# Kernel tuning notes

Measured on AMD Instinct MI355X. Metric: run time of the kernel, lower is better.

## Reference

```python
import jax, jax.numpy as jnp
import numpy as np

B, N, DIM, HEADS = 2, 2048, 1024, 16
DH = DIM // HEADS
SCALE = DH ** -0.5


def setup_inputs() -> dict:
    key = jax.random.key(0)
    k1, k2, k3, k4 = jax.random.split(key, 4)
    x = jax.random.normal(k1, (B, N, DIM), dtype=jnp.float32)
    # nn.Linear weights stored as [out, in]; apply as x @ W.T
    w_qkv = jax.random.normal(k2, (3 * DIM, DIM), dtype=jnp.float32) * (DIM ** -0.5)
    w_out = jax.random.normal(k3, (DIM, DIM), dtype=jnp.float32) * (DIM ** -0.5)
    b_out = jax.random.normal(k4, (DIM,), dtype=jnp.float32) * 0.01
    return {"x": x, "w_qkv": w_qkv, "w_out": w_out, "b_out": b_out}


def reference(x, w_qkv, w_out, b_out):
    b, n, _ = x.shape
    qkv = jnp.einsum('bnd,ed->bne', x, w_qkv)  # [b, n, 3*dim]
    q, k, v = jnp.split(qkv, 3, axis=-1)
    # [b, n, dim] -> [b, heads, n, dim_head]
    def split_heads(t):
        return t.reshape(b, n, HEADS, DH).transpose(0, 2, 1, 3)
    q, k, v = split_heads(q), split_heads(k), split_heads(v)
    attn = jnp.einsum('bhid,bhjd->bhij', q, k) * SCALE  # [b, h, n, n]
    attn = jax.nn.softmax(attn, axis=-1)
    out = jnp.einsum('bhij,bhjd->bhid', attn, v)  # [b, h, n, dh]
    out = out.transpose(0, 2, 1, 3).reshape(b, n, DIM)
    return jnp.einsum('bnd,ed->bne', out, w_out) + b_out
```

## Files before the change

### kernel.cpp

```cpp
#include <hip/hip_runtime.h>
#include <hip/hip_bf16.h>
#include <stdint.h>

#define BB 2
#define NN 2048
#define DIMM 1024
#define HEADS 16
#define DH 64
#define E3 3072
#define LOG2E_ 1.44269504088896f
#define THR_ 8.0f

typedef __bf16 bf16;
typedef __attribute__((ext_vector_type(8))) __bf16 bf16x8;
typedef __attribute__((ext_vector_type(4))) __bf16 bf16x4;
typedef __attribute__((ext_vector_type(4))) float f32x4;

__device__ __forceinline__ void gload_lds16(const void* gsrc, void* ldst) {
  __builtin_amdgcn_global_load_lds(
      (const __attribute__((address_space(1))) uint32_t*)(uintptr_t)gsrc,
      (__attribute__((address_space(3))) uint32_t*)(uintptr_t)ldst,
      16, 0, 0);
}

__global__ __launch_bounds__(256)
void convert_all(const float* __restrict__ x, const float* __restrict__ wqkv,
                 const float* __restrict__ wout,
                 bf16* __restrict__ xb, bf16* __restrict__ wqb, bf16* __restrict__ wob) {
  size_t i = (size_t)blockIdx.x * blockDim.x + threadIdx.x;
  const float* src;
  bf16* dst;
  size_t off;
  if (i < 1048576u) { src = x; dst = xb; off = i; }
  else if (i < 1048576u + 786432u) { src = wqkv; dst = wqb; off = i - 1048576u; }
  else { src = wout; dst = wob; off = i - (1048576u + 786432u); }
  float4 v = ((const float4*)src)[off];
  bf16x4 o;
  o[0] = (bf16)v.x; o[1] = (bf16)v.y; o[2] = (bf16)v.z; o[3] = (bf16)v.w;
  *(bf16x4*)(dst + off * 4) = o;
}

#define GDSR(dst, base, off) \
  asm volatile("ds_read_b128 %0, %1 offset:%c2" : "=v"(dst) : "v"(base), "i"(off))

#define GRD12(ABASE, BBASE, OFF) \
  GDSR(af0, ABASE, (OFF));        GDSR(af1, ABASE, (OFF)+2048); \
  GDSR(af2, ABASE, (OFF)+4096);   GDSR(af3, ABASE, (OFF)+6144); \
  GDSR(af4, ABASE, (OFF)+8192);   GDSR(af5, ABASE, (OFF)+10240); \
  GDSR(af6, ABASE, (OFF)+12288);  GDSR(af7, ABASE, (OFF)+14336); \
  GDSR(bf0, BBASE, (OFF));        GDSR(bf1, BBASE, (OFF)+2048); \
  GDSR(bf2, BBASE, (OFF)+4096);   GDSR(bf3, BBASE, (OFF)+6144);

#define GMM32() \
  acc[0][0]=__builtin_amdgcn_mfma_f32_16x16x32_bf16(af0,bf0,acc[0][0],0,0,0); \
  acc[0][1]=__builtin_amdgcn_mfma_f32_16x16x32_bf16(af0,bf1,acc[0][1],0,0,0); \
  acc[0][2]=__builtin_amdgcn_mfma_f32_16x16x32_bf16(af0,bf2,acc[0][2],0,0,0); \
  acc[0][3]=__builtin_amdgcn_mfma_f32_16x16x32_bf16(af0,bf3,acc[0][3],0,0,0); \
  acc[1][0]=__builtin_amdgcn_mfma_f32_16x16x32_bf16(af1,bf0,acc[1][0],0,0,0); \
  acc[1][1]=__builtin_amdgcn_mfma_f32_16x16x32_bf16(af1,bf1,acc[1][1],0,0,0); \
  acc[1][2]=__builtin_amdgcn_mfma_f32_16x16x32_bf16(af1,bf2,acc[1][2],0,0,0); \
  acc[1][3]=__builtin_amdgcn_mfma_f32_16x16x32_bf16(af1,bf3,acc[1][3],0,0,0); \
  acc[2][0]=__builtin_amdgcn_mfma_f32_16x16x32_bf16(af2,bf0,acc[2][0],0,0,0); \
  acc[2][1]=__builtin_amdgcn_mfma_f32_16x16x32_bf16(af2,bf1,acc[2][1],0,0,0); \
  acc[2][2]=__builtin_amdgcn_mfma_f32_16x16x32_bf16(af2,bf2,acc[2][2],0,0,0); \
  acc[2][3]=__builtin_amdgcn_mfma_f32_16x16x32_bf16(af2,bf3,acc[2][3],0,0,0); \
  acc[3][0]=__builtin_amdgcn_mfma_f32_16x16x32_bf16(af3,bf0,acc[3][0],0,0,0); \
  acc[3][1]=__builtin_amdgcn_mfma_f32_16x16x32_bf16(af3,bf1,acc[3][1],0,0,0); \
  acc[3][2]=__builtin_amdgcn_mfma_f32_16x16x32_bf16(af3,bf2,acc[3][2],0,0,0); \
  acc[3][3]=__builtin_amdgcn_mfma_f32_16x16x32_bf16(af3,bf3,acc[3][3],0,0,0); \
  acc[4][0]=__builtin_amdgcn_mfma_f32_16x16x32_bf16(af4,bf0,acc[4][0],0,0,0); \
  acc[4][1]=__builtin_amdgcn_mfma_f32_16x16x32_bf16(af4,bf1,acc[4][1],0,0,0); \
  acc[4][2]=__builtin_amdgcn_mfma_f32_16x16x32_bf16(af4,bf2,acc[4][2],0,0,0); \
  acc[4][3]=__builtin_amdgcn_mfma_f32_16x16x32_bf16(af4,bf3,acc[4][3],0,0,0); \
  acc[5][0]=__builtin_amdgcn_mfma_f32_16x16x32_bf16(af5,bf0,acc[5][0],0,0,0); \
  acc[5][1]=__builtin_amdgcn_mfma_f32_16x16x32_bf16(af5,bf1,acc[5][1],0,0,0); \
  acc[5][2]=__builtin_amdgcn_mfma_f32_16x16x32_bf16(af5,bf2,acc[5][2],0,0,0); \
  acc[5][3]=__builtin_amdgcn_mfma_f32_16x16x32_bf16(af5,bf3,acc[5][3],0,0,0); \
  acc[6][0]=__builtin_amdgcn_mfma_f32_16x16x32_bf16(af6,bf0,acc[6][0],0,0,0); \
  acc[6][1]=__builtin_amdgcn_mfma_f32_16x16x32_bf16(af6,bf1,acc[6][1],0,0,0); \
  acc[6][2]=__builtin_amdgcn_mfma_f32_16x16x32_bf16(af6,bf2,acc[6][2],0,0,0); \
  acc[6][3]=__builtin_amdgcn_mfma_f32_16x16x32_bf16(af6,bf3,acc[6][3],0,0,0); \
  acc[7][0]=__builtin_amdgcn_mfma_f32_16x16x32_bf16(af7,bf0,acc[7][0],0,0,0); \
  acc[7][1]=__builtin_amdgcn_mfma_f32_16x16x32_bf16(af7,bf1,acc[7][1],0,0,0); \
  acc[7][2]=__builtin_amdgcn_mfma_f32_16x16x32_bf16(af7,bf2,acc[7][2],0,0,0); \
  acc[7][3]=__builtin_amdgcn_mfma_f32_16x16x32_bf16(af7,bf3,acc[7][3],0,0,0);

#define GSTAGE(BUF) { \
  gload_lds16(pA,          smem + (BUF)*32768 + w*1024); \
  gload_lds16(pA + 65536,  smem + (BUF)*32768 + 8192 + w*1024); \
  gload_lds16(pA + 131072, smem + (BUF)*32768 + 16384 + w*1024); \
  gload_lds16(pA + 196608, smem + (BUF)*32768 + 24576 + w*1024); \
  gload_lds16(pB,          smem + 65536 + (BUF)*32768 + w*1024); \
  gload_lds16(pB + 65536,  smem + 65536 + (BUF)*32768 + 8192 + w*1024); \
  gload_lds16(pB + 131072, smem + 65536 + (BUF)*32768 + 16384 + w*1024); \
  gload_lds16(pB + 196608, smem + 65536 + (BUF)*32768 + 24576 + w*1024); \
  pA += 64; pB += 64; }

#define GSTEP(BUF, DOSTAGE) { \
  bf16x8 af0, af1, af2, af3, af4, af5, af6, af7, bf0, bf1, bf2, bf3; \
  GRD12(abase0, bbase0, (BUF)*32768); \
  if (DOSTAGE) { GSTAGE((BUF)^1); } \
  asm volatile("s_waitcnt lgkmcnt(0)" ::: "memory"); \
  __builtin_amdgcn_sched_barrier(0); \
  __builtin_amdgcn_s_setprio(1); \
  GMM32(); \
  __builtin_amdgcn_s_setprio(0); \
  GRD12(abase1, bbase1, (BUF)*32768); \
  asm volatile("s_waitcnt lgkmcnt(0)" ::: "memory"); \
  __builtin_amdgcn_sched_barrier(0); \
  __builtin_amdgcn_s_setprio(1); \
  GMM32(); \
  __builtin_amdgcn_s_setprio(0); \
  if (DOSTAGE) { asm volatile("s_waitcnt vmcnt(0)" ::: "memory"); } \
  __builtin_amdgcn_sched_barrier(0); \
  __builtin_amdgcn_s_barrier(); \
}

__global__ __launch_bounds__(512, 2)
void gemm_qkv(const bf16* __restrict__ A, const bf16* __restrict__ Bw,
              bf16* __restrict__ C) {
  int bid = blockIdx.x;
  bid = (bid & 7) * 24 + (bid >> 3);
  const int nx = bid % 12;
  const int ny = bid / 12;
  const int m0 = ny * 256, n0 = nx * 256;
  const int tid = threadIdx.x;
  const int w = tid >> 6, lane = tid & 63, c = lane & 15, g = lane >> 4;
  const int wr = w >> 2, wc = w & 3;

  __shared__ __align__(16) char smem[131072];
  const uint32_t smem32 = (uint32_t)(uintptr_t)smem;
  const uint32_t abase0 = smem32 + (wr * 128 + c) * 128 + ((g ^ (c & 7)) * 16);
  const uint32_t abase1 = smem32 + (wr * 128 + c) * 128 + (((4 + g) ^ (c & 7)) * 16);
  const uint32_t bbase0 = smem32 + 65536 + (wc * 64 + c) * 128 + ((g ^ (c & 7)) * 16);
  const uint32_t bbase1 = smem32 + 65536 + (wc * 64 + c) * 128 + (((4 + g) ^ (c & 7)) * 16);

  const bf16 *pA, *pB;
  {
    const int r0 = tid >> 3;
    const int cc = (tid & 7) ^ ((tid >> 3) & 7);
    pA = A + (size_t)(m0 + r0) * 1024 + cc * 8;
    pB = Bw + (size_t)(n0 + r0) * 1024 + cc * 8;
  }

  f32x4 acc[8][4] = {};

  GSTAGE(0);
  asm volatile("s_waitcnt vmcnt(0)" ::: "memory");
  __builtin_amdgcn_sched_barrier(0);
  __builtin_amdgcn_s_barrier();

  for (int u = 0; u < 7; ++u) {
    GSTEP(0, 1) GSTEP(1, 1)
  }
  GSTEP(0, 1)
  GSTEP(1, 0)

  const float qsc = (n0 < 1024) ? 0.125f : 1.0f;
#pragma unroll
  for (int fr = 0; fr < 8; ++fr) {
    const int row = m0 + wr * 128 + fr * 16 + g * 4;
#pragma unroll
    for (int fc = 0; fc < 4; ++fc) {
      const int col = n0 + wc * 64 + fc * 16 + c;
#pragma unroll
      for (int r = 0; r < 4; ++r)
        C[(size_t)(row + r) * E3 + col] = (bf16)(acc[fr][fc][r] * qsc);
    }
  }
}

template <int OUTMODE>
__global__ __launch_bounds__(256)
void gemm_bt(const bf16* __restrict__ A, const bf16* __restrict__ Bw,
             void* __restrict__ Cout, const float* __restrict__ bias, int ldc) {
  const int tid = threadIdx.x;
  const int w = tid >> 6;
  const int lane = tid & 63;
  const int c = lane & 15;
  const int g = lane >> 4;
  const int wr = w >> 1, wc = w & 1;
  const int m0 = blockIdx.y * 128;
  const int n0 = blockIdx.x * 128;

  __shared__ __align__(16) char smem[16384];
  char* As = smem;
  char* Bs = smem + 8192;

  f32x4 acc[4][4] = {};

  for (int kt = 0; kt < 1024; kt += 32) {
    __syncthreads();
#pragma unroll
    for (int it = 0; it < 2; ++it) {
      int t = it * 256 + tid;
      int row = t >> 2, cc = t & 3;
      gload_lds16(A + (size_t)(m0 + row) * 1024 + kt + cc * 8, As + it * 4096 + w * 1024);
      gload_lds16(Bw + (size_t)(n0 + row) * 1024 + kt + cc * 8, Bs + it * 4096 + w * 1024);
    }
    __syncthreads();

    bf16x8 af[4], bfr[4];
#pragma unroll
    for (int i = 0; i < 4; ++i)
      af[i] = *(const bf16x8*)(As + ((wr * 64 + i * 16 + c) * 32 + g * 8) * 2);
#pragma unroll
    for (int j = 0; j < 4; ++j)
      bfr[j] = *(const bf16x8*)(Bs + ((wc * 64 + j * 16 + c) * 32 + g * 8) * 2);
#pragma unroll
    for (int i = 0; i < 4; ++i)
#pragma unroll
      for (int j = 0; j < 4; ++j)
        acc[i][j] = __builtin_amdgcn_mfma_f32_16x16x32_bf16(af[i], bfr[j], acc[i][j], 0, 0, 0);
  }

  if (OUTMODE == 0) {
    const float qsc = (n0 < 1024) ? 0.125f : 1.0f;
    bf16* Cc = (bf16*)Cout;
#pragma unroll
    for (int i = 0; i < 4; ++i) {
      int row = m0 + wr * 64 + i * 16 + g * 4;
#pragma unroll
      for (int j = 0; j < 4; ++j) {
        int col = n0 + wc * 64 + j * 16 + c;
#pragma unroll
        for (int r = 0; r < 4; ++r)
          Cc[(size_t)(row + r) * ldc + col] = (bf16)(acc[i][j][r] * qsc);
      }
    }
  } else {
    float* Cc = (float*)Cout;
#pragma unroll
    for (int i = 0; i < 4; ++i) {
      int row = m0 + wr * 64 + i * 16 + g * 4;
#pragma unroll
      for (int j = 0; j < 4; ++j) {
        int col = n0 + wc * 64 + j * 16 + c;
        float bv = bias[col];
#pragma unroll
        for (int r = 0; r < 4; ++r)
          Cc[(size_t)(row + r) * ldc + col] = acc[i][j][r] + bv;
      }
    }
  }
}

#define DSR128(dst, base, off) \
  asm volatile("ds_read_b128 %0, %1 offset:%c2" : "=v"(dst) : "v"(base), "i"(off))
#define DSTR(dst, base, off) \
  asm volatile("ds_read_b64_tr_b16 %0, %1 offset:%c2" : "=v"(dst) : "v"(base), "i"(off))

#define KF_ALL(KB) \
  DSR128(kf[0][0], kb0, (KB)*8192 + 0);    DSR128(kf[0][1], kb1, (KB)*8192 + 0); \
  DSR128(kf[1][0], kb0, (KB)*8192 + 2048); DSR128(kf[1][1], kb1, (KB)*8192 + 2048); \
  DSR128(kf[2][0], kb0, (KB)*8192 + 4096); DSR128(kf[2][1], kb1, (KB)*8192 + 4096); \
  DSR128(kf[3][0], kb0, (KB)*8192 + 6144); DSR128(kf[3][1], kb1, (KB)*8192 + 6144);

#define TRPAIR(f, ks, VP) \
  DSTR(tlo[f][ks], tb, (VP)*8192 + (f)*2048 + (ks)*1024); \
  DSTR(thi[f][ks], tb, (VP)*8192 + (f)*2048 + (ks)*1024 + 512);
#define TR_ALL(VP) \
  TRPAIR(0,0,VP) TRPAIR(0,1,VP) TRPAIR(1,0,VP) TRPAIR(1,1,VP) \
  TRPAIR(2,0,VP) TRPAIR(2,1,VP) TRPAIR(3,0,VP) TRPAIR(3,1,VP)

#define SMAX_A(SPRV, qc) { \
  f32x4 vm = SPRV[0][qc]; \
  _Pragma("unroll") for (int j = 1; j < 4; ++j) \
    _Pragma("unroll") for (int r = 0; r < 4; ++r) vm[r] = fmaxf(vm[r], SPRV[j][qc][r]); \
  float rmax = fmaxf(fmaxf(vm[0], vm[1]), fmaxf(vm[2], vm[3])); \
  rmax = fmaxf(rmax, __shfl_xor(rmax, 16, 64)); \
  rmax = fmaxf(rmax, __shfl_xor(rmax, 32, 64)); \
  const float rmax2 = rmax * LOG2E_; \
  if (!__all(rmax2 <= mrun[qc] + THR_)) { \
    const float mnew = fmaxf(mrun[qc], rmax2); \
    const float fac = __builtin_amdgcn_exp2f(mrun[qc] - mnew); \
    mrun[qc] = mnew; \
    _Pragma("unroll") for (int f = 0; f < 4; ++f) oacc[f][qc] *= fac; \
    lacc[qc] *= fac; \
  } }

#define SMAX_B(SPRV, qc) { \
  const float negm = -mrun[qc]; \
  f32x4 p[4]; \
  _Pragma("unroll") for (int j = 0; j < 4; ++j) \
    _Pragma("unroll") for (int r = 0; r < 4; ++r) \
      p[j][r] = __builtin_amdgcn_exp2f(fmaf(SPRV[j][qc][r], LOG2E_, negm)); \
  _Pragma("unroll") for (int ks = 0; ks < 2; ++ks) \
    _Pragma("unroll") for (int r = 0; r < 4; ++r) { \
      vb[qc][ks][r] = (bf16)p[ks][r]; vb[qc][ks][4 + r] = (bf16)p[ks + 2][r]; \
    } }

#define QK_ALL(SCUR) \
  _Pragma("unroll") for (int j = 0; j < 4; ++j) { \
    f32x4 z = {0.f, 0.f, 0.f, 0.f}; \
    f32x4 s0 = __builtin_amdgcn_mfma_f32_16x16x32_bf16(kf[j][0], qf[0][0], z, 0, 0, 0); \
    s0 = __builtin_amdgcn_mfma_f32_16x16x32_bf16(kf[j][1], qf[0][1], s0, 0, 0, 0); \
    SCUR[j][0] = s0; \
    f32x4 s1 = __builtin_amdgcn_mfma_f32_16x16x32_bf16(kf[j][0], qf[1][0], z, 0, 0, 0); \
    s1 = __builtin_amdgcn_mfma_f32_16x16x32_bf16(kf[j][1], qf[1][1], s1, 0, 0, 0); \
    SCUR[j][1] = s1; }

#define PV_ALL() \
  _Pragma("unroll") for (int f = 0; f < 4; ++f) \
    _Pragma("unroll") for (int ks = 0; ks < 2; ++ks) { \
      bf16x8 va; \
      _Pragma("unroll") for (int e = 0; e < 4; ++e) { va[e] = tlo[f][ks][e]; va[4+e] = thi[f][ks][e]; } \
      oacc[f][0] = __builtin_amdgcn_mfma_f32_16x16x32_bf16(va, vb[0][ks], oacc[f][0], 0, 0, 0); \
      oacc[f][1] = __builtin_amdgcn_mfma_f32_16x16x32_bf16(va, vb[1][ks], oacc[f][1], 0, 0, 0); \
    } \
  lacc[0] = __builtin_amdgcn_mfma_f32_16x16x32_bf16(ones, vb[0][0], lacc[0], 0, 0, 0); \
  lacc[0] = __builtin_amdgcn_mfma_f32_16x16x32_bf16(ones, vb[0][1], lacc[0], 0, 0, 0); \
  lacc[1] = __builtin_amdgcn_mfma_f32_16x16x32_bf16(ones, vb[1][0], lacc[1], 0, 0, 0); \
  lacc[1] = __builtin_amdgcn_mfma_f32_16x16x32_bf16(ones, vb[1][1], lacc[1], 0, 0, 0);

#define STEP(KB, VN, VP, SCUR, SPRV, DOSTAGE, DOPREV) { \
  if (DOSTAGE) { \
    gload_lds16(pK0, smem + ((KB)^1)*8192 + w*1024); \
    gload_lds16(pK1, smem + ((KB)^1)*8192 + 4096 + w*1024); \
    gload_lds16(pV0, smem + 16384 + (VN)*8192 + w*1024); \
    gload_lds16(pV1, smem + 16384 + (VN)*8192 + 4096 + w*1024); \
    pK0 += 64*E3; pK1 += 64*E3; pV0 += 64*E3; pV1 += 64*E3; \
  } \
  if (DOPREV) { SMAX_A(SPRV, 0); SMAX_A(SPRV, 1); } \
  __builtin_amdgcn_sched_barrier(0); \
  KF_ALL(KB); \
  if (DOPREV) { TR_ALL(VP); } \
  if (DOPREV) { SMAX_B(SPRV, 0); SMAX_B(SPRV, 1); } \
  if (DOPREV) { asm volatile("s_waitcnt lgkmcnt(15)" ::: "memory"); } \
  else        { asm volatile("s_waitcnt lgkmcnt(0)" ::: "memory"); } \
  __builtin_amdgcn_sched_barrier(0); \
  __builtin_amdgcn_s_setprio(1); \
  QK_ALL(SCUR); \
  __builtin_amdgcn_s_setprio(0); \
  if (DOPREV) { \
    asm volatile("s_waitcnt lgkmcnt(0)" ::: "memory"); \
    __builtin_amdgcn_sched_barrier(0); \
    __builtin_amdgcn_s_setprio(1); \
    PV_ALL(); \
    __builtin_amdgcn_s_setprio(0); \
  } \
  __syncthreads(); \
}

__global__ __launch_bounds__(256, 2)
void flash_attn(const bf16* __restrict__ qkv, bf16* __restrict__ attb) {
  int bid = blockIdx.x;
  bid = (bid & 7) * 64 + (bid >> 3);
  const int tid = threadIdx.x;
  const int w = tid >> 6;
  const int lane = tid & 63;
  const int c = lane & 15;
  const int g = lane >> 4;
  const int qt = bid & 15;
  const int bh = bid >> 4;
  const int b = bh >> 4;
  const int h = bh & 15;
  const int q0 = qt * 128 + w * 32;

  __shared__ __align__(16) char smem[49152];
  const uint32_t smem32 = (uint32_t)(uintptr_t)smem;

  const uint32_t kb0 = smem32 + c * 128 + ((g ^ (c & 7)) * 16);
  const uint32_t kb1 = smem32 + c * 128 + (((4 + g) ^ (c & 7)) * 16);
  const uint32_t tb  = smem32 + 16384 + lane * 8;

  bf16x8 qf[2][2];
#pragma unroll
  for (int qc = 0; qc < 2; ++qc) {
    const size_t qbase = (size_t)(b * NN + q0 + qc * 16 + c) * E3 + h * 64;
    qf[qc][0] = *(const bf16x8*)(qkv + qbase + g * 8);
    qf[qc][1] = *(const bf16x8*)(qkv + qbase + 32 + g * 8);
  }

  bf16x8 ones;
#pragma unroll
  for (int e = 0; e < 8; ++e) ones[e] = (bf16)1.0f;

  const bf16 *pK0, *pK1, *pV0, *pV1;
  {
    int tK0 = tid, tK1 = 256 + tid;
    int r0 = tK0 >> 3, s0 = (tK0 & 7) ^ (r0 & 7);
    int r1 = tK1 >> 3, s1 = (tK1 & 7) ^ (r1 & 7);
    pK0 = qkv + (size_t)(b * NN + r0) * E3 + 1024 + h * 64 + s0 * 8;
    pK1 = qkv + (size_t)(b * NN + r1) * E3 + 1024 + h * 64 + s1 * 8;
    int sv0 = tid, sv1 = 256 + tid;
    int f0 = sv0 >> 7, ks0 = (sv0 >> 6) & 1, o0 = (sv0 >> 5) & 1,
        g0 = (sv0 >> 3) & 3, j0 = (sv0 >> 1) & 3, i0 = sv0 & 1;
    int f1 = sv1 >> 7, ks1 = (sv1 >> 6) & 1, o1 = (sv1 >> 5) & 1,
        g1 = (sv1 >> 3) & 3, j1 = (sv1 >> 1) & 3, i1 = sv1 & 1;
    int key0 = 32 * o0 + 16 * ks0 + 4 * g0 + j0;
    int key1 = 32 * o1 + 16 * ks1 + 4 * g1 + j1;
    pV0 = qkv + (size_t)(b * NN + key0) * E3 + 2048 + h * 64 + f0 * 16 + i0 * 8;
    pV1 = qkv + (size_t)(b * NN + key1) * E3 + 2048 + h * 64 + f1 * 16 + i1 * 8;
  }

  f32x4 oacc[4][2] = {};
  f32x4 lacc[2] = {};
  float mrun[2] = {-1e30f, -1e30f};
  f32x4 sA[4][2], sB[4][2];
  bf16x8 kf[4][2];
  bf16x4 tlo[4][2], thi[4][2];
  bf16x8 vb[2][2];

  gload_lds16(pK0, smem + w * 1024);
  gload_lds16(pK1, smem + 4096 + w * 1024);
  gload_lds16(pV0, smem + 16384 + w * 1024);
  gload_lds16(pV1, smem + 16384 + 4096 + w * 1024);
  pK0 += 64 * E3; pK1 += 64 * E3; pV0 += 64 * E3; pV1 += 64 * E3;
  __syncthreads();

  STEP(0, 1, 0, sA, sB, 1, 0)
  for (int to = 1; to <= 25; to += 4) {
    STEP(1, 2, 0, sB, sA, 1, 1)
    STEP(0, 3, 1, sA, sB, 1, 1)
    STEP(1, 0, 2, sB, sA, 1, 1)
    STEP(0, 1, 3, sA, sB, 1, 1)
  }
  STEP(1, 2, 0, sB, sA, 1, 1)
  STEP(0, 3, 1, sA, sB, 1, 1)
  STEP(1, 0, 2, sB, sA, 0, 1)

  SMAX_A(sB, 0); SMAX_A(sB, 1);
  TR_ALL(3);
  SMAX_B(sB, 0); SMAX_B(sB, 1);
  asm volatile("s_waitcnt lgkmcnt(0)" ::: "memory");
  __builtin_amdgcn_sched_barrier(0);
  PV_ALL();

#pragma unroll
  for (int qc = 0; qc < 2; ++qc) {
    const float inv = __builtin_amdgcn_rcpf(lacc[qc][0]);
    const size_t row = (size_t)(b * NN + q0 + qc * 16 + c);
#pragma unroll
    for (int f = 0; f < 4; ++f) {
      bf16x4 o;
#pragma unroll
      for (int r = 0; r < 4; ++r) o[r] = (bf16)(oacc[f][qc][r] * inv);
      *(bf16x4*)(attb + row * 1024 + h * 64 + f * 16 + 4 * g) = o;
    }
  }
}

extern "C" void kernel_launch(void* const* d_in, const int* in_sizes, int n_in,
                              void* d_out, int out_size, void* d_ws, size_t ws_size,
                              hipStream_t stream) {
  const float* x = (const float*)d_in[0];
  const float* wqkv = (const float*)d_in[1];
  const float* wout = (const float*)d_in[2];
  const float* bout = (const float*)d_in[3];

  char* ws = (char*)d_ws;
  bf16* xb   = (bf16*)(ws);
  bf16* wqb  = (bf16*)(ws + 8388608);
  bf16* wob  = (bf16*)(ws + 14680064);
  bf16* qkvb = (bf16*)(ws + 16777216);
  bf16* attb = (bf16*)(ws + 41943040);

  convert_all<<<8192, 256, 0, stream>>>(x, wqkv, wout, xb, wqb, wob);
  gemm_qkv<<<192, 512, 0, stream>>>(xb, wqb, qkvb);
  flash_attn<<<512, 256, 0, stream>>>(qkvb, attb);
  gemm_bt<1><<<dim3(8, 32), 256, 0, stream>>>(attb, wob, d_out, bout, DIMM);
}
```

Measured before the change: 110.9 us.

## Rewrite output projection GEMM with double-buffered LDS pipeline and swizzled layout

Replaces the simple output-projection GEMM, which syncs twice per K=32 step, with a double-buffered kernel over K=64 tiles. The next tile's global-to-LDS load overlaps with the MFMAs on the current one, and LDS rows get an XOR swizzle to avoid bank conflicts. It also remaps block IDs for better L2 locality and raises MFMA priority around the compute bursts. The kernel uses 64KB of LDS and relies on hand-placed waitcnt and barriers, which adds register pressure and makes correctness depend on getting that ordering right.

```diff
diff --git a/kernel.cpp b/kernel.cpp
--- a/kernel.cpp
+++ b/kernel.cpp
@@ -170,77 +170,111 @@
   }
 }
 
-template <int OUTMODE>
-__global__ __launch_bounds__(256)
-void gemm_bt(const bf16* __restrict__ A, const bf16* __restrict__ Bw,
-             void* __restrict__ Cout, const float* __restrict__ bias, int ldc) {
+#define ORD8(ABASE, BBASE, OFF) \
+  GDSR(ao0, ABASE, (OFF));        GDSR(ao1, ABASE, (OFF)+2048); \
+  GDSR(ao2, ABASE, (OFF)+4096);   GDSR(ao3, ABASE, (OFF)+6144); \
+  GDSR(bo0, BBASE, (OFF));        GDSR(bo1, BBASE, (OFF)+2048); \
+  GDSR(bo2, BBASE, (OFF)+4096);   GDSR(bo3, BBASE, (OFF)+6144);
+
+#define OMM16() \
+  acc[0][0]=__builtin_amdgcn_mfma_f32_16x16x32_bf16(ao0,bo0,acc[0][0],0,0,0); \
+  acc[0][1]=__builtin_amdgcn_mfma_f32_16x16x32_bf16(ao0,bo1,acc[0][1],0,0,0); \
+  acc[0][2]=__builtin_amdgcn_mfma_f32_16x16x32_bf16(ao0,bo2,acc[0][2],0,0,0); \
+  acc[0][3]=__builtin_amdgcn_mfma_f32_16x16x32_bf16(ao0,bo3,acc[0][3],0,0,0); \
+  acc[1][0]=__builtin_amdgcn_mfma_f32_16x16x32_bf16(ao1,bo0,acc[1][0],0,0,0); \
+  acc[1][1]=__builtin_amdgcn_mfma_f32_16x16x32_bf16(ao1,bo1,acc[1][1],0,0,0); \
+  acc[1][2]=__builtin_amdgcn_mfma_f32_16x16x32_bf16(ao1,bo2,acc[1][2],0,0,0); \
+  acc[1][3]=__builtin_amdgcn_mfma_f32_16x16x32_bf16(ao1,bo3,acc[1][3],0,0,0); \
+  acc[2][0]=__builtin_amdgcn_mfma_f32_16x16x32_bf16(ao2,bo0,acc[2][0],0,0,0); \
+  acc[2][1]=__builtin_amdgcn_mfma_f32_16x16x32_bf16(ao2,bo1,acc[2][1],0,0,0); \
+  acc[2][2]=__builtin_amdgcn_mfma_f32_16x16x32_bf16(ao2,bo2,acc[2][2],0,0,0); \
+  acc[2][3]=__builtin_amdgcn_mfma_f32_16x16x32_bf16(ao2,bo3,acc[2][3],0,0,0); \
+  acc[3][0]=__builtin_amdgcn_mfma_f32_16x16x32_bf16(ao3,bo0,acc[3][0],0,0,0); \
+  acc[3][1]=__builtin_amdgcn_mfma_f32_16x16x32_bf16(ao3,bo1,acc[3][1],0,0,0); \
+  acc[3][2]=__builtin_amdgcn_mfma_f32_16x16x32_bf16(ao3,bo2,acc[3][2],0,0,0); \
+  acc[3][3]=__builtin_amdgcn_mfma_f32_16x16x32_bf16(ao3,bo3,acc[3][3],0,0,0);
+
+#define OSTAGE(BUF) { \
+  gload_lds16(pA,          smem + (BUF)*16384 + w*1024); \
+  gload_lds16(pA + 32768,  smem + (BUF)*16384 + 4096 + w*1024); \
+  gload_lds16(pA + 65536,  smem + (BUF)*16384 + 8192 + w*1024); \
+  gload_lds16(pA + 98304,  smem + (BUF)*16384 + 12288 + w*1024); \
+  gload_lds16(pB,          smem + 32768 + (BUF)*16384 + w*1024); \
+  gload_lds16(pB + 32768,  smem + 32768 + (BUF)*16384 + 4096 + w*1024); \
+  gload_lds16(pB + 65536,  smem + 32768 + (BUF)*16384 + 8192 + w*1024); \
+  gload_lds16(pB + 98304,  smem + 32768 + (BUF)*16384 + 12288 + w*1024); \
+  pA += 64; pB += 64; }
+
+#define OSTEP(BUF, DOSTAGE) { \
+  bf16x8 ao0, ao1, ao2, ao3, bo0, bo1, bo2, bo3; \
+  ORD8(abase0, bbase0, (BUF)*16384); \
+  if (DOSTAGE) { OSTAGE((BUF)^1); } \
+  asm volatile("s_waitcnt lgkmcnt(0)" ::: "memory"); \
+  __builtin_amdgcn_sched_barrier(0); \
+  __builtin_amdgcn_s_setprio(1); \
+  OMM16(); \
+  __builtin_amdgcn_s_setprio(0); \
+  ORD8(abase1, bbase1, (BUF)*16384); \
+  asm volatile("s_waitcnt lgkmcnt(0)" ::: "memory"); \
+  __builtin_amdgcn_sched_barrier(0); \
+  __builtin_amdgcn_s_setprio(1); \
+  OMM16(); \
+  __builtin_amdgcn_s_setprio(0); \
+  if (DOSTAGE) { asm volatile("s_waitcnt vmcnt(0)" ::: "memory"); } \
+  __builtin_amdgcn_sched_barrier(0); \
+  __builtin_amdgcn_s_barrier(); \
+}
+
+__global__ __launch_bounds__(256, 2)
+void gemm_out(const bf16* __restrict__ A, const bf16* __restrict__ Bw,
+              float* __restrict__ C, const float* __restrict__ bias) {
+  int bid = blockIdx.x;
+  bid = (bid & 7) * 32 + (bid >> 3);
+  const int nx = bid & 7;
+  const int ny = bid >> 3;
+  const int m0 = ny * 128, n0 = nx * 128;
   const int tid = threadIdx.x;
-  const int w = tid >> 6;
-  const int lane = tid & 63;
-  const int c = lane & 15;
-  const int g = lane >> 4;
+  const int w = tid >> 6, lane = tid & 63, c = lane & 15, g = lane >> 4;
   const int wr = w >> 1, wc = w & 1;
-  const int m0 = blockIdx.y * 128;
-  const int n0 = blockIdx.x * 128;
-
-  __shared__ __align__(16) char smem[16384];
-  char* As = smem;
-  char* Bs = smem + 8192;
+
+  __shared__ __align__(16) char smem[65536];
+  const uint32_t smem32 = (uint32_t)(uintptr_t)smem;
+  const uint32_t abase0 = smem32 + (wr * 64 + c) * 128 + ((g ^ (c & 7)) * 16);
+  const uint32_t abase1 = smem32 + (wr * 64 + c) * 128 + (((4 + g) ^ (c & 7)) * 16);
+  const uint32_t bbase0 = smem32 + 32768 + (wc * 64 + c) * 128 + ((g ^ (c & 7)) * 16);
+  const uint32_t bbase1 = smem32 + 32768 + (wc * 64 + c) * 128 + (((4 + g) ^ (c & 7)) * 16);
+
+  const bf16 *pA, *pB;
+  {
+    const int r0 = tid >> 3;
+    const int cc = (tid & 7) ^ ((tid >> 3) & 7);
+    pA = A + (size_t)(m0 + r0) * 1024 + cc * 8;
+    pB = Bw + (size_t)(n0 + r0) * 1024 + cc * 8;
+  }
 
   f32x4 acc[4][4] = {};
 
-  for (int kt = 0; kt < 1024; kt += 32) {
-    __syncthreads();
-#pragma unroll
-    for (int it = 0; it < 2; ++it) {
-      int t = it * 256 + tid;
-      int row = t >> 2, cc = t & 3;
-      gload_lds16(A + (size_t)(m0 + row) * 1024 + kt + cc * 8, As + it * 4096 + w * 1024);
-      gload_lds16(Bw + (size_t)(n0 + row) * 1024 + kt + cc * 8, Bs + it * 4096 + w * 1024);
-    }
-    __syncthreads();
-
-    bf16x8 af[4], bfr[4];
-#pragma unroll
-    for (int i = 0; i < 4; ++i)
-      af[i] = *(const bf16x8*)(As + ((wr * 64 + i * 16 + c) * 32 + g * 8) * 2);
-#pragma unroll
-    for (int j = 0; j < 4; ++j)
-      bfr[j] = *(const bf16x8*)(Bs + ((wc * 64 + j * 16 + c) * 32 + g * 8) * 2);
-#pragma unroll
-    for (int i = 0; i < 4; ++i)
-#pragma unroll
-      for (int j = 0; j < 4; ++j)
-        acc[i][j] = __builtin_amdgcn_mfma_f32_16x16x32_bf16(af[i], bfr[j], acc[i][j], 0, 0, 0);
-  }
-
-  if (OUTMODE == 0) {
-    const float qsc = (n0 < 1024) ? 0.125f : 1.0f;
-    bf16* Cc = (bf16*)Cout;
-#pragma unroll
-    for (int i = 0; i < 4; ++i) {
-      int row = m0 + wr * 64 + i * 16 + g * 4;
-#pragma unroll
-      for (int j = 0; j < 4; ++j) {
-        int col = n0 + wc * 64 + j * 16 + c;
-#pragma unroll
-        for (int r = 0; r < 4; ++r)
-          Cc[(size_t)(row + r) * ldc + col] = (bf16)(acc[i][j][r] * qsc);
-      }
-    }
-  } else {
-    float* Cc = (float*)Cout;
-#pragma unroll
-    for (int i = 0; i < 4; ++i) {
-      int row = m0 + wr * 64 + i * 16 + g * 4;
-#pragma unroll
-      for (int j = 0; j < 4; ++j) {
-        int col = n0 + wc * 64 + j * 16 + c;
-        float bv = bias[col];
-#pragma unroll
-        for (int r = 0; r < 4; ++r)
-          Cc[(size_t)(row + r) * ldc + col] = acc[i][j][r] + bv;
-      }
+  OSTAGE(0);
+  asm volatile("s_waitcnt vmcnt(0)" ::: "memory");
+  __builtin_amdgcn_sched_barrier(0);
+  __builtin_amdgcn_s_barrier();
+
+  for (int u = 0; u < 7; ++u) {
+    OSTEP(0, 1) OSTEP(1, 1)
+  }
+  OSTEP(0, 1)
+  OSTEP(1, 0)
+
+#pragma unroll
+  for (int i = 0; i < 4; ++i) {
+    const int row = m0 + wr * 64 + i * 16 + g * 4;
+#pragma unroll
+    for (int j = 0; j < 4; ++j) {
+      const int col = n0 + wc * 64 + j * 16 + c;
+      const float bv = bias[col];
+#pragma unroll
+      for (int r = 0; r < 4; ++r)
+        C[(size_t)(row + r) * DIMM + col] = acc[i][j][r] + bv;
     }
   }
 }
@@ -459,5 +493,5 @@
   convert_all<<<8192, 256, 0, stream>>>(x, wqkv, wout, xb, wqb, wob);
   gemm_qkv<<<192, 512, 0, stream>>>(xb, wqb, qkvb);
   flash_attn<<<512, 256, 0, stream>>>(qkvb, attb);
-  gemm_bt<1><<<dim3(8, 32), 256, 0, stream>>>(attb, wob, d_out, bout, DIMM);
-}
+  gemm_out<<<256, 256, 0, stream>>>(attb, wob, (float*)d_out, bout);
+}
```

After: 106.6 us. 1.04x faster.
